# Performance work log

Measured on AMD Instinct MI355X. Metric: run time of the kernel, lower is better.

Reference implementation:

```python
import jax, jax.numpy as jnp
import numpy as np

N_NODES = 50000
N_EDGES = 800000
IN_DIM = 128
HID = 64
N_LAYERS = 3


def setup_inputs() -> dict:
    key = jax.random.key(0)
    ks = jax.random.split(key, 12)
    x = jax.random.normal(ks[0], (N_NODES, IN_DIM), dtype=jnp.float32)
    edge_index = jax.random.randint(ks[1], (2, N_EDGES), 0, N_NODES, dtype=jnp.int64)
    s = 0.05
    Wp = jax.random.normal(ks[2], (IN_DIM, HID), dtype=jnp.float32) * s
    bp = jax.random.normal(ks[3], (HID,), dtype=jnp.float32) * s
    # per-layer EdgeConv MLP params, stacked over layers
    W1 = jax.random.normal(ks[4], (N_LAYERS, 2 * HID, HID), dtype=jnp.float32) * s
    b1 = jax.random.normal(ks[5], (N_LAYERS, HID), dtype=jnp.float32) * s
    W2 = jax.random.normal(ks[6], (N_LAYERS, HID, HID), dtype=jnp.float32) * s
    b2 = jax.random.normal(ks[7], (N_LAYERS, HID), dtype=jnp.float32) * s
    Wo = jax.random.normal(ks[8], (HID, 1), dtype=jnp.float32) * s
    bo = jax.random.normal(ks[9], (1,), dtype=jnp.float32) * s
    return {"x": x, "edge_index": edge_index, "Wp": Wp, "bp": bp,
            "W1": W1, "b1": b1, "W2": W2, "b2": b2, "Wo": Wo, "bo": bo}


def _edge_conv(h, src, dst, W1, b1, W2, b2):
    # PyG EdgeConv: message = MLP(cat[x_i, x_j - x_i]), aggr = max over incoming edges
    xi = h[dst]                       # [E, H] center (target) features
    xj = h[src]                       # [E, H] neighbor (source) features
    e = jnp.concatenate([xi, xj - xi], axis=-1)   # [E, 2H]
    m = jnp.maximum(e @ W1 + b1, 0.0) @ W2 + b2   # [E, H]
    agg = jax.ops.segment_max(m, dst, num_segments=N_NODES)  # [N, H]
    # nodes with no incoming edges get 0 (PyG scatter-max fill value)
    return jnp.where(jnp.isfinite(agg), agg, 0.0)


def reference(x, edge_index, Wp, bp, W1, b1, W2, b2, Wo, bo):
    src, dst = edge_index[0], edge_index[1]
    h = x @ Wp + bp                   # input projection [N, H]
    for l in range(N_LAYERS):
        residual = h
        h = _edge_conv(h, src, dst, W1[l], b1[l], W2[l], b2[l])
        h = jnp.maximum(h, 0.0)       # relu; dropout is identity in eval
        h = h + residual
    return (h @ Wo + bo)[:, 0]        # squeeze(-1) -> [N]
```

## Files before the change

### kernel.cpp

```cpp
#include <hip/hip_runtime.h>

#define NN 50000
#define IN_DIM 128
#define HID 64
#define NLAYERS 3
#define PART_SZ 6250

typedef __attribute__((ext_vector_type(8))) short bf16x8;
typedef __attribute__((ext_vector_type(4))) float f32x4;

__device__ __forceinline__ unsigned f2bf(float f) {
    unsigned u = __float_as_uint(f);
    return (u + 0x7fffu + ((u >> 16) & 1u)) >> 16;
}

__device__ __forceinline__ unsigned pk2bf(float a, float b) {
    return __builtin_amdgcn_perm(__float_as_uint(b) + 0x8000u,
                                 __float_as_uint(a) + 0x8000u, 0x07060302u);
}

__device__ __forceinline__ unsigned pack_r(unsigned q, float pA, float pB) {
    float lo = fmaxf(__uint_as_float(q << 16) + pA, 0.f);
    float hi = fmaxf(__uint_as_float(q & 0xffff0000u) + pB, 0.f);
    return pk2bf(lo, hi);
}

__global__ void k_zero(int* __restrict__ p, int n) {
    int i = blockIdx.x * blockDim.x + threadIdx.x;
    if (i < n) p[i] = 0;
}

__global__ void __launch_bounds__(256) k_count_part(const int* __restrict__ dst,
                                                    int* __restrict__ deg, int E) {
    int lo = (blockIdx.x & 7) * PART_SZ, hi = lo + PART_SZ;
    int stride = (gridDim.x >> 3) * 256;
    for (int e = (blockIdx.x >> 3) * 256 + threadIdx.x; e < E; e += stride) {
        int d = dst[e];
        if (d >= lo && d < hi) atomicAdd(&deg[d], 1);
    }
}

__global__ void k_scan_partial(const int* __restrict__ deg, int* __restrict__ part, int n) {
    __shared__ int s[256];
    int i = blockIdx.x * 256 + threadIdx.x;
    s[threadIdx.x] = (i < n) ? deg[i] : 0;
    __syncthreads();
    for (int d = 128; d > 0; d >>= 1) {
        if (threadIdx.x < d) s[threadIdx.x] += s[threadIdx.x + d];
        __syncthreads();
    }
    if (threadIdx.x == 0) part[blockIdx.x] = s[0];
}

__global__ void k_scan_root(int* part, int nb) {
    __shared__ int s[256];
    int t = threadIdx.x;
    int v = (t < nb) ? part[t] : 0;
    s[t] = v;
    __syncthreads();
    for (int d = 1; d < 256; d <<= 1) {
        int add = (t >= d) ? s[t - d] : 0;
        __syncthreads();
        s[t] += add;
        __syncthreads();
    }
    if (t < nb) part[t] = s[t] - v;
}

__global__ void k_scan_final(const int* __restrict__ deg, const int* __restrict__ part,
                             int* __restrict__ off, int2* __restrict__ meta, int n) {
    __shared__ int s[256];
    int t = threadIdx.x;
    int i = blockIdx.x * 256 + t;
    int v = (i < n) ? deg[i] : 0;
    s[t] = v;
    __syncthreads();
    for (int d = 1; d < 256; d <<= 1) {
        int add = (t >= d) ? s[t - d] : 0;
        __syncthreads();
        s[t] += add;
        __syncthreads();
    }
    if (i < n) {
        int o = part[blockIdx.x] + s[t] - v;
        off[i] = o;
        meta[i] = make_int2(o, v);
    }
}

__global__ void __launch_bounds__(256) k_scatter_part(
    const int* __restrict__ src, const int* __restrict__ dst,
    const int* __restrict__ off, int* __restrict__ cursor,
    unsigned short* __restrict__ csr, int E) {
    int lo = (blockIdx.x & 7) * PART_SZ, hi = lo + PART_SZ;
    int stride = (gridDim.x >> 3) * 256;
    for (int e = (blockIdx.x >> 3) * 256 + threadIdx.x; e < E; e += stride) {
        int d = dst[e];
        if (d >= lo && d < hi) {
            int pos = atomicAdd(&cursor[d], 1);
            csr[off[d] + pos] = (unsigned short)src[e];
        }
    }
}

__global__ void __launch_bounds__(256) k_projpq(
    const float* __restrict__ x, const float* __restrict__ Wp,
    const float* __restrict__ bp, const float* __restrict__ W1,
    const float* __restrict__ b1, float* __restrict__ h,
    float* __restrict__ P, unsigned short* __restrict__ Qb) {
    __shared__ float hs[4][16][66];
    int lane = threadIdx.x & 63, wave = threadIdx.x >> 6;
    int col = lane & 15, quad = lane >> 4;
    int node0 = (blockIdx.x * 4 + wave) * 16;
    if (node0 >= NN) return;

    bf16x8 bw[4][4];
#pragma unroll
    for (int t = 0; t < 4; t++)
#pragma unroll
        for (int kc = 0; kc < 4; kc++) {
            uint4 u;
#pragma unroll
            for (int jp = 0; jp < 4; jp++) {
                int k0 = kc * 32 + quad * 8 + jp * 2;
                ((unsigned*)&u)[jp] = pk2bf(Wp[k0 * HID + t * 16 + col],
                                            Wp[(k0 + 1) * HID + t * 16 + col]);
            }
            bw[t][kc] = __builtin_bit_cast(bf16x8, u);
        }
    const float4* xr = (const float4*)(x + (size_t)(node0 + col) * IN_DIM);
    bf16x8 ax[4];
#pragma unroll
    for (int kc = 0; kc < 4; kc++) {
        float4 f0 = xr[kc * 8 + quad * 2], f1 = xr[kc * 8 + quad * 2 + 1];
        uint4 u;
        u.x = pk2bf(f0.x, f0.y); u.y = pk2bf(f0.z, f0.w);
        u.z = pk2bf(f1.x, f1.y); u.w = pk2bf(f1.z, f1.w);
        ax[kc] = __builtin_bit_cast(bf16x8, u);
    }
#pragma unroll
    for (int t = 0; t < 4; t++) {
        f32x4 c = (f32x4)(0.f);
#pragma unroll
        for (int kc = 0; kc < 4; kc++)
            c = __builtin_amdgcn_mfma_f32_16x16x32_bf16(ax[kc], bw[t][kc], c, 0, 0, 0);
        float bv = bp[t * 16 + col];
#pragma unroll
        for (int r = 0; r < 4; r++) {
            float hv = c[r] + bv;
            int row = quad * 4 + r;
            h[(size_t)(node0 + row) * HID + t * 16 + col] = hv;
            hs[wave][row][t * 16 + col] = hv;
        }
    }

    bf16x8 bfr[8][2];
#pragma unroll
    for (int t = 0; t < 8; t++)
#pragma unroll
        for (int hf = 0; hf < 2; hf++) {
            uint4 u;
#pragma unroll
            for (int jp = 0; jp < 4; jp++) {
                int k0 = hf * 32 + quad * 8 + jp * 2;
                float w0, w1v;
                if (t < 4) {
                    int n = t * 16 + col;
                    w0  = W1[k0 * HID + n] - W1[(HID + k0) * HID + n];
                    w1v = W1[(k0 + 1) * HID + n] - W1[(HID + k0 + 1) * HID + n];
                } else {
                    int n = (t - 4) * 16 + col;
                    w0  = W1[(HID + k0) * HID + n];
                    w1v = W1[(HID + k0 + 1) * HID + n];
                }
                ((unsigned*)&u)[jp] = pk2bf(w0, w1v);
            }
            bfr[t][hf] = __builtin_bit_cast(bf16x8, u);
        }
    const float* hl = &hs[wave][col][0];
    uint4 au, bu;
    {
        float2 e0 = *(const float2*)(hl + quad * 8);
        float2 e1 = *(const float2*)(hl + quad * 8 + 2);
        float2 e2 = *(const float2*)(hl + quad * 8 + 4);
        float2 e3 = *(const float2*)(hl + quad * 8 + 6);
        au.x = pk2bf(e0.x, e0.y); au.y = pk2bf(e1.x, e1.y);
        au.z = pk2bf(e2.x, e2.y); au.w = pk2bf(e3.x, e3.y);
        float2 f0 = *(const float2*)(hl + 32 + quad * 8);
        float2 f1 = *(const float2*)(hl + 32 + quad * 8 + 2);
        float2 f2 = *(const float2*)(hl + 32 + quad * 8 + 4);
        float2 f3 = *(const float2*)(hl + 32 + quad * 8 + 6);
        bu.x = pk2bf(f0.x, f0.y); bu.y = pk2bf(f1.x, f1.y);
        bu.z = pk2bf(f2.x, f2.y); bu.w = pk2bf(f3.x, f3.y);
    }
    bf16x8 a0 = __builtin_bit_cast(bf16x8, au);
    bf16x8 a1 = __builtin_bit_cast(bf16x8, bu);
#pragma unroll
    for (int t = 0; t < 8; t++) {
        f32x4 c = __builtin_amdgcn_mfma_f32_16x16x32_bf16(a0, bfr[t][0], (f32x4)(0.f), 0, 0, 0);
        c = __builtin_amdgcn_mfma_f32_16x16x32_bf16(a1, bfr[t][1], c, 0, 0, 0);
        if (t < 4) {
            float bv = b1[t * 16 + col];
#pragma unroll
            for (int r = 0; r < 4; r++)
                P[(size_t)(node0 + quad * 4 + r) * HID + t * 16 + col] = c[r] + bv;
        } else {
#pragma unroll
            for (int r = 0; r < 4; r++)
                Qb[(size_t)(node0 + quad * 4 + r) * HID + (t - 4) * 16 + col] =
                    (unsigned short)f2bf(c[r]);
        }
    }
}

__global__ void __launch_bounds__(256) k_pq_mfma(
    const float* __restrict__ h, const float* __restrict__ W1,
    const float* __restrict__ b1, float* __restrict__ P,
    unsigned short* __restrict__ Qb, int layer) {
    int lane = threadIdx.x & 63, wave = threadIdx.x >> 6;
    int col = lane & 15, quad = lane >> 4;
    int node0 = (blockIdx.x * 4 + wave) * 16;
    if (node0 >= NN) return;
    const float* W1l = W1 + layer * 2 * HID * HID;

    bf16x8 bfr[8][2];
#pragma unroll
    for (int t = 0; t < 8; t++)
#pragma unroll
        for (int hf = 0; hf < 2; hf++) {
            uint4 u;
#pragma unroll
            for (int jp = 0; jp < 4; jp++) {
                int k0 = hf * 32 + quad * 8 + jp * 2;
                float w0, w1v;
                if (t < 4) {
                    int n = t * 16 + col;
                    w0  = W1l[k0 * HID + n] - W1l[(HID + k0) * HID + n];
                    w1v = W1l[(k0 + 1) * HID + n] - W1l[(HID + k0 + 1) * HID + n];
                } else {
                    int n = (t - 4) * 16 + col;
                    w0  = W1l[(HID + k0) * HID + n];
                    w1v = W1l[(HID + k0 + 1) * HID + n];
                }
                ((unsigned*)&u)[jp] = pk2bf(w0, w1v);
            }
            bfr[t][hf] = __builtin_bit_cast(bf16x8, u);
        }

    const float* hrow = h + (size_t)(node0 + col) * HID;
    float4 ha0 = *(const float4*)(hrow + quad * 8);
    float4 ha1 = *(const float4*)(hrow + quad * 8 + 4);
    float4 hb0 = *(const float4*)(hrow + 32 + quad * 8);
    float4 hb1 = *(const float4*)(hrow + 32 + quad * 8 + 4);
    uint4 au, bu;
    au.x = pk2bf(ha0.x, ha0.y); au.y = pk2bf(ha0.z, ha0.w);
    au.z = pk2bf(ha1.x, ha1.y); au.w = pk2bf(ha1.z, ha1.w);
    bu.x = pk2bf(hb0.x, hb0.y); bu.y = pk2bf(hb0.z, hb0.w);
    bu.z = pk2bf(hb1.x, hb1.y); bu.w = pk2bf(hb1.z, hb1.w);
    bf16x8 a0 = __builtin_bit_cast(bf16x8, au);
    bf16x8 a1 = __builtin_bit_cast(bf16x8, bu);

#pragma unroll
    for (int t = 0; t < 8; t++) {
        f32x4 c = __builtin_amdgcn_mfma_f32_16x16x32_bf16(a0, bfr[t][0], (f32x4)(0.f), 0, 0, 0);
        c = __builtin_amdgcn_mfma_f32_16x16x32_bf16(a1, bfr[t][1], c, 0, 0, 0);
        if (t < 4) {
            float bv = b1[layer * HID + t * 16 + col];
#pragma unroll
            for (int r = 0; r < 4; r++)
                P[(size_t)(node0 + quad * 4 + r) * HID + t * 16 + col] = c[r] + bv;
        } else {
#pragma unroll
            for (int r = 0; r < 4; r++)
                Qb[(size_t)(node0 + quad * 4 + r) * HID + (t - 4) * 16 + col] =
                    (unsigned short)f2bf(c[r]);
        }
    }
}

__global__ void __launch_bounds__(256) k_edge(
    const float* __restrict__ P, const unsigned short* __restrict__ Qb,
    const float* __restrict__ W2, const float* __restrict__ b2,
    const int2* __restrict__ meta, const unsigned short* __restrict__ csr,
    float* __restrict__ h, int layer, int nw,
    int fin, const float* __restrict__ Wo, const float* __restrict__ bo,
    float* __restrict__ outp) {
    __shared__ uint4 qstage[4][16][9];
    int lane = threadIdx.x & 63;
    int col = lane & 15, quad = lane >> 4;
    int wave = threadIdx.x >> 6;
    int rrow = lane >> 3, sseg = lane & 7;
    int wid = (blockIdx.x * blockDim.x + threadIdx.x) >> 6;

    const float* W2l = W2 + layer * HID * HID;
    bf16x8 bfr[4][2];
#pragma unroll
    for (int t = 0; t < 4; t++)
#pragma unroll
        for (int hf = 0; hf < 2; hf++) {
            uint4 u;
#pragma unroll
            for (int jp = 0; jp < 4; jp++) {
                int k0 = hf * 32 + quad * 8 + jp * 2;
                ((unsigned*)&u)[jp] = pk2bf(W2l[k0 * HID + t * 16 + col],
                                            W2l[(k0 + 1) * HID + t * 16 + col]);
            }
            bfr[t][hf] = __builtin_bit_cast(bf16x8, u);
        }
    float b2v = b2[layer * HID + lane];
    float wov = fin ? Wo[lane] : 0.f;

    for (int node = wid; node < NN; node += nw) {
        int2 md = meta[node];
        int start = __builtin_amdgcn_readfirstlane(md.x);
        int cnt   = __builtin_amdgcn_readfirstlane(md.y);
        float res = h[(size_t)node * HID + lane];
        float outv = 0.f;
        if (cnt > 0) {
            const float4* prow = (const float4*)(P + (size_t)node * HID);
            float4 pA = prow[quad * 2], pB = prow[quad * 2 + 1];
            float4 pC = prow[8 + quad * 2], pD = prow[8 + quad * 2 + 1];
            f32x4 mx[4];
#pragma unroll
            for (int t = 0; t < 4; t++) mx[t] = (f32x4)(-3.4e38f);
            for (int b0 = 0; b0 < cnt; b0 += 16) {
                int e1 = b0 + rrow, e2 = b0 + 8 + rrow;
                int s1 = csr[start + (e1 < cnt ? e1 : b0)];
                int s2 = csr[start + (e2 < cnt ? e2 : b0)];
                uint4 v1 = ((const uint4*)(Qb + (size_t)s1 * HID))[sseg];
                uint4 v2 = ((const uint4*)(Qb + (size_t)s2 * HID))[sseg];
                qstage[wave][rrow][sseg] = v1;
                qstage[wave][8 + rrow][sseg] = v2;
                uint4 q0 = qstage[wave][col][quad];
                uint4 q1 = qstage[wave][col][4 + quad];
                uint4 a0u, a1u;
                a0u.x = pack_r(q0.x, pA.x, pA.y);
                a0u.y = pack_r(q0.y, pA.z, pA.w);
                a0u.z = pack_r(q0.z, pB.x, pB.y);
                a0u.w = pack_r(q0.w, pB.z, pB.w);
                a1u.x = pack_r(q1.x, pC.x, pC.y);
                a1u.y = pack_r(q1.y, pC.z, pC.w);
                a1u.z = pack_r(q1.z, pD.x, pD.y);
                a1u.w = pack_r(q1.w, pD.z, pD.w);
                bf16x8 a0 = __builtin_bit_cast(bf16x8, a0u);
                bf16x8 a1 = __builtin_bit_cast(bf16x8, a1u);
#pragma unroll
                for (int t = 0; t < 4; t++) {
                    f32x4 c = __builtin_amdgcn_mfma_f32_16x16x32_bf16(
                        a0, bfr[t][0], (f32x4)(0.f), 0, 0, 0);
                    c = __builtin_amdgcn_mfma_f32_16x16x32_bf16(
                        a1, bfr[t][1], c, 0, 0, 0);
#pragma unroll
                    for (int r = 0; r < 4; r++)
                        mx[t][r] = fmaxf(mx[t][r], c[r]);
                }
            }
            float v[4];
#pragma unroll
            for (int t = 0; t < 4; t++) {
                v[t] = fmaxf(fmaxf(mx[t][0], mx[t][1]), fmaxf(mx[t][2], mx[t][3]));
                v[t] = fmaxf(v[t], __shfl_xor(v[t], 16, 64));
                v[t] = fmaxf(v[t], __shfl_xor(v[t], 32, 64));
            }
            float vs = quad == 0 ? v[0] : quad == 1 ? v[1] : quad == 2 ? v[2] : v[3];
            outv = fmaxf(vs + b2v, 0.f);
        }
        float hv = outv + res;
        h[(size_t)node * HID + lane] = hv;
        if (fin) {
            float v = hv * wov;
#pragma unroll
            for (int m = 32; m >= 1; m >>= 1) v += __shfl_xor(v, m, 64);
            if (lane == 0) outp[node] = v + bo[0];
        }
    }
}

extern "C" void kernel_launch(void* const* d_in, const int* in_sizes, int n_in,
                              void* d_out, int out_size, void* d_ws, size_t ws_size,
                              hipStream_t stream) {
    const float* x  = (const float*)d_in[0];
    const int*   ei = (const int*)d_in[1];
    const float* Wp = (const float*)d_in[2];
    const float* bp = (const float*)d_in[3];
    const float* W1 = (const float*)d_in[4];
    const float* b1 = (const float*)d_in[5];
    const float* W2 = (const float*)d_in[6];
    const float* b2 = (const float*)d_in[7];
    const float* Wo = (const float*)d_in[8];
    const float* bo = (const float*)d_in[9];
    float* out = (float*)d_out;

    const int E = in_sizes[1] / 2;
    const int N = NN;
    const int* srcp = ei;
    const int* dstp = ei + E;

    float* h  = (float*)d_ws;
    float* Pb = h + (size_t)N * HID;
    unsigned short* Qb = (unsigned short*)(Pb + (size_t)N * HID);
    int* deg    = (int*)(Qb + (size_t)N * HID);
    int* cursor = deg + N;
    int* off    = cursor + N;
    int* part   = off + N;
    int2* meta  = (int2*)(part + 256);
    unsigned short* csr = (unsigned short*)(meta + N);

    int nbN = (N + 255) / 256;

    k_zero<<<(2 * N + 255) / 256, 256, 0, stream>>>(deg, 2 * N);
    k_count_part<<<512, 256, 0, stream>>>(dstp, deg, E);
    k_scan_partial<<<nbN, 256, 0, stream>>>(deg, part, N);
    k_scan_root<<<1, 256, 0, stream>>>(part, nbN);
    k_scan_final<<<nbN, 256, 0, stream>>>(deg, part, off, meta, N);
    k_scatter_part<<<512, 256, 0, stream>>>(srcp, dstp, off, cursor, csr, E);

    const int PQ_BLOCKS = (N / 16 + 3) / 4;
    k_projpq<<<PQ_BLOCKS, 256, 0, stream>>>(x, Wp, bp, W1, b1, h, Pb, Qb);

    const int EDGE_BLOCKS = 2048;
    const int NW = EDGE_BLOCKS * 256 / 64;
    for (int l = 0; l < NLAYERS; l++) {
        if (l > 0)
            k_pq_mfma<<<PQ_BLOCKS, 256, 0, stream>>>(h, W1, b1, Pb, Qb, l);
        k_edge<<<EDGE_BLOCKS, 256, 0, stream>>>(Pb, Qb, W2, b2, meta, csr, h, l, NW,
                                                l == NLAYERS - 1 ? 1 : 0, Wo, bo, out);
    }
}
```

Measured before the change: 351.4 us.

## Build CSR via two-level bucket sort with LDS histograms instead of global atomics

Replaces the global-atomic degree count, three-kernel scan and partitioned global-atomic scatter with a bucketed sort. Edges are grouped into 32-node bins using per-chunk LDS histograms and an LDS-cursor scatter into a scratch buffer, then each bin is counting-sorted in LDS to produce the CSR and per-node metadata. This removes contended global atomics and the repeated full passes over dst that the 8-way partitioning needed. In exchange the histogram and scatter kernels launch only 32 blocks, which leaves most of the GPU idle. The per-bin sort also assumes no bin holds more than 1024 edges, which only holds for roughly uniform inputs.

```diff
diff --git a/kernel.cpp b/kernel.cpp
--- a/kernel.cpp
+++ b/kernel.cpp
@@ -4,7 +4,8 @@
 #define IN_DIM 128
 #define HID 64
 #define NLAYERS 3
-#define PART_SZ 6250
+#define NB 1563
+#define CHUNKS 32
 
 typedef __attribute__((ext_vector_type(8))) short bf16x8;
 typedef __attribute__((ext_vector_type(4))) float f32x4;
@@ -25,83 +26,106 @@
     return pk2bf(lo, hi);
 }
 
-__global__ void k_zero(int* __restrict__ p, int n) {
-    int i = blockIdx.x * blockDim.x + threadIdx.x;
-    if (i < n) p[i] = 0;
-}
-
-__global__ void __launch_bounds__(256) k_count_part(const int* __restrict__ dst,
-                                                    int* __restrict__ deg, int E) {
-    int lo = (blockIdx.x & 7) * PART_SZ, hi = lo + PART_SZ;
-    int stride = (gridDim.x >> 3) * 256;
-    for (int e = (blockIdx.x >> 3) * 256 + threadIdx.x; e < E; e += stride) {
-        int d = dst[e];
-        if (d >= lo && d < hi) atomicAdd(&deg[d], 1);
-    }
-}
-
-__global__ void k_scan_partial(const int* __restrict__ deg, int* __restrict__ part, int n) {
-    __shared__ int s[256];
-    int i = blockIdx.x * 256 + threadIdx.x;
-    s[threadIdx.x] = (i < n) ? deg[i] : 0;
-    __syncthreads();
-    for (int d = 128; d > 0; d >>= 1) {
-        if (threadIdx.x < d) s[threadIdx.x] += s[threadIdx.x + d];
-        __syncthreads();
-    }
-    if (threadIdx.x == 0) part[blockIdx.x] = s[0];
-}
-
-__global__ void k_scan_root(int* part, int nb) {
+
+__global__ void __launch_bounds__(256) k_hist32(const int* __restrict__ dst,
+                                                int* __restrict__ cnt32, int E, int CE) {
+    __shared__ int lh[NB];
+    int g = blockIdx.x;
+    for (int i = threadIdx.x; i < NB; i += 256) lh[i] = 0;
+    __syncthreads();
+    int e0 = g * CE, e1 = min(E, e0 + CE);
+    for (int e = e0 + threadIdx.x; e < e1; e += 256) atomicAdd(&lh[dst[e] >> 5], 1);
+    __syncthreads();
+    for (int i = threadIdx.x; i < NB; i += 256) cnt32[g * NB + i] = lh[i];
+}
+
+__global__ void k_base(const int* __restrict__ cnt32, int* __restrict__ base32,
+                       int* __restrict__ bincnt) {
+    int b = blockIdx.x * 256 + threadIdx.x;
+    if (b < NB) {
+        int run = 0;
+#pragma unroll 4
+        for (int g = 0; g < CHUNKS; g++) {
+            base32[g * NB + b] = run;
+            run += cnt32[g * NB + b];
+        }
+        bincnt[b] = run;
+    }
+}
+
+__global__ void k_binscan(const int* __restrict__ bincnt, int* __restrict__ binoff) {
     __shared__ int s[256];
     int t = threadIdx.x;
-    int v = (t < nb) ? part[t] : 0;
-    s[t] = v;
-    __syncthreads();
-    for (int d = 1; d < 256; d <<= 1) {
-        int add = (t >= d) ? s[t - d] : 0;
+    int carry = 0;
+    for (int c0 = 0; c0 < NB; c0 += 256) {
+        int v = (c0 + t < NB) ? bincnt[c0 + t] : 0;
+        s[t] = v;
         __syncthreads();
-        s[t] += add;
+        for (int d = 1; d < 256; d <<= 1) {
+            int a = (t >= d) ? s[t - d] : 0;
+            __syncthreads();
+            s[t] += a;
+            __syncthreads();
+        }
+        if (c0 + t < NB) binoff[c0 + t] = carry + s[t] - v;
+        carry += s[255];
         __syncthreads();
     }
-    if (t < nb) part[t] = s[t] - v;
-}
-
-__global__ void k_scan_final(const int* __restrict__ deg, const int* __restrict__ part,
-                             int* __restrict__ off, int2* __restrict__ meta, int n) {
-    __shared__ int s[256];
-    int t = threadIdx.x;
-    int i = blockIdx.x * 256 + t;
-    int v = (i < n) ? deg[i] : 0;
-    s[t] = v;
-    __syncthreads();
-    for (int d = 1; d < 256; d <<= 1) {
-        int add = (t >= d) ? s[t - d] : 0;
-        __syncthreads();
-        s[t] += add;
-        __syncthreads();
-    }
-    if (i < n) {
-        int o = part[blockIdx.x] + s[t] - v;
-        off[i] = o;
-        meta[i] = make_int2(o, v);
-    }
-}
-
-__global__ void __launch_bounds__(256) k_scatter_part(
+}
+
+__global__ void __launch_bounds__(256) k_scatter32(
     const int* __restrict__ src, const int* __restrict__ dst,
-    const int* __restrict__ off, int* __restrict__ cursor,
-    unsigned short* __restrict__ csr, int E) {
-    int lo = (blockIdx.x & 7) * PART_SZ, hi = lo + PART_SZ;
-    int stride = (gridDim.x >> 3) * 256;
-    for (int e = (blockIdx.x >> 3) * 256 + threadIdx.x; e < E; e += stride) {
+    const int* __restrict__ base32, const int* __restrict__ binoff,
+    unsigned* __restrict__ bscratch, int E, int CE) {
+    __shared__ int cur[NB];
+    int g = blockIdx.x;
+    for (int i = threadIdx.x; i < NB; i += 256)
+        cur[i] = binoff[i] + base32[g * NB + i];
+    __syncthreads();
+    int e0 = g * CE, e1 = min(E, e0 + CE);
+    for (int e = e0 + threadIdx.x; e < e1; e += 256) {
         int d = dst[e];
-        if (d >= lo && d < hi) {
-            int pos = atomicAdd(&cursor[d], 1);
-            csr[off[d] + pos] = (unsigned short)src[e];
-        }
-    }
-}
+        int pos = atomicAdd(&cur[d >> 5], 1);
+        bscratch[pos] = ((unsigned)(d & 31) << 16) | (unsigned)src[e];
+    }
+}
+
+__global__ void __launch_bounds__(256) k_binsort(
+    const unsigned* __restrict__ bscratch, const int* __restrict__ bincnt,
+    const int* __restrict__ binoff, unsigned short* __restrict__ csr,
+    int2* __restrict__ meta) {
+    __shared__ unsigned entries[1024];
+    __shared__ unsigned short sorted[1024];
+    __shared__ int cnt[32];
+    int bin = blockIdx.x, t = threadIdx.x;
+    int n = bincnt[bin], boff = binoff[bin];
+    for (int i = t; i < n; i += 256) entries[i] = bscratch[boff + i];
+    if (t < 32) cnt[t] = 0;
+    __syncthreads();
+    for (int i = t; i < n; i += 256) atomicAdd(&cnt[entries[i] >> 16], 1);
+    __syncthreads();
+    if (t < 32) {
+        int c = cnt[t];
+        int s = c;
+#pragma unroll
+        for (int d = 1; d < 32; d <<= 1) {
+            int o = __shfl_up(s, d, 64);
+            if (t >= d) s += o;
+        }
+        int node = bin * 32 + t;
+        if (node < NN) meta[node] = make_int2(boff + s - c, c);
+        cnt[t] = s - c;
+    }
+    __syncthreads();
+    for (int i = t; i < n; i += 256) {
+        unsigned e = entries[i];
+        int p = atomicAdd(&cnt[e >> 16], 1);
+        sorted[p] = (unsigned short)(e & 0xffffu);
+    }
+    __syncthreads();
+    for (int i = t; i < n; i += 256) csr[boff + i] = sorted[i];
+}
+
 
 __global__ void __launch_bounds__(256) k_projpq(
     const float* __restrict__ x, const float* __restrict__ Wp,
@@ -399,21 +423,21 @@
     float* h  = (float*)d_ws;
     float* Pb = h + (size_t)N * HID;
     unsigned short* Qb = (unsigned short*)(Pb + (size_t)N * HID);
-    int* deg    = (int*)(Qb + (size_t)N * HID);
-    int* cursor = deg + N;
-    int* off    = cursor + N;
-    int* part   = off + N;
-    int2* meta  = (int2*)(part + 256);
-    unsigned short* csr = (unsigned short*)(meta + N);
-
-    int nbN = (N + 255) / 256;
-
-    k_zero<<<(2 * N + 255) / 256, 256, 0, stream>>>(deg, 2 * N);
-    k_count_part<<<512, 256, 0, stream>>>(dstp, deg, E);
-    k_scan_partial<<<nbN, 256, 0, stream>>>(deg, part, N);
-    k_scan_root<<<1, 256, 0, stream>>>(part, nbN);
-    k_scan_final<<<nbN, 256, 0, stream>>>(deg, part, off, meta, N);
-    k_scatter_part<<<512, 256, 0, stream>>>(srcp, dstp, off, cursor, csr, E);
+    int* cnt32  = (int*)(Qb + (size_t)N * HID);
+    int* base32 = cnt32 + CHUNKS * NB;
+    int* bincnt = base32 + CHUNKS * NB;
+    int* binoff = bincnt + NB;
+    int2* meta  = (int2*)(binoff + NB);
+    unsigned* bscratch = (unsigned*)(meta + N);
+    unsigned short* csr = (unsigned short*)(bscratch + E);
+
+    const int CE = (E + CHUNKS - 1) / CHUNKS;
+
+    k_hist32<<<CHUNKS, 256, 0, stream>>>(dstp, cnt32, E, CE);
+    k_base<<<(NB + 255) / 256, 256, 0, stream>>>(cnt32, base32, bincnt);
+    k_binscan<<<1, 256, 0, stream>>>(bincnt, binoff);
+    k_scatter32<<<CHUNKS, 256, 0, stream>>>(srcp, dstp, base32, binoff, bscratch, E, CE);
+    k_binsort<<<NB, 256, 0, stream>>>(bscratch, bincnt, binoff, csr, meta);
 
     const int PQ_BLOCKS = (N / 16 + 3) / 4;
     k_projpq<<<PQ_BLOCKS, 256, 0, stream>>>(x, Wp, bp, W1, b1, h, Pb, Qb);
```

Result: slower. 361.5 us (+2.9%).
